# Kernel tuning notes

Measured on AMD Instinct MI355X. Metric: run time of the kernel, lower is better.

## Reference

```python
import jax, jax.numpy as jnp
from jax import lax
import numpy as np

NUM_CLASSES = 7
EDGE_LO, EDGE_HI = 2, 7  # edge_classes = [2,3,4,5,6]
FOCAL_W, DICE_W, BOUND_W, TOPO_W = 0.3, 0.3, 0.2, 0.2
GAMMA = 2.0


def _dwconv(x, k):
    # depthwise 'same' conv with identical spatial kernel per channel
    C = x.shape[1]
    kern = jnp.broadcast_to(k[None, None], (C, 1) + k.shape)
    return lax.conv_general_dilated(
        x, kern, (1, 1), 'SAME',
        dimension_numbers=('NCHW', 'OIHW', 'NCHW'),
        feature_group_count=C)


def setup_inputs() -> dict:
    key = jax.random.key(0)
    k1, k2 = jax.random.split(key)
    logits = jax.random.normal(k1, (8, NUM_CLASSES, 512, 512), dtype=jnp.float32)
    targets = jax.random.randint(k2, (8, 512, 512), 0, NUM_CLASSES, dtype=jnp.int32)
    class_weights = jnp.ones((NUM_CLASSES,), dtype=jnp.float32)
    return {"logits": logits, "targets": targets, "class_weights": class_weights}


def reference(logits, targets, class_weights):
    C = logits.shape[1]
    logp = jax.nn.log_softmax(logits, axis=1)          # [B,C,H,W]
    probs = jnp.exp(logp)
    onehot = (targets[:, None, :, :] == jnp.arange(C)[None, :, None, None]).astype(logits.dtype)

    # ---- Focal loss (weighted CE, pt from the *weighted* CE as in torch code) ----
    nll = -jnp.take_along_axis(logp, targets[:, None].astype(jnp.int32), axis=1)[:, 0]  # [B,H,W]
    ce = class_weights[targets] * nll
    pt = jnp.exp(-ce)
    loss_focal = jnp.mean((1.0 - pt) ** GAMMA * ce)

    # ---- Dice loss (per class, global sums) ----
    inter = jnp.sum(probs * onehot, axis=(0, 2, 3))    # [C]
    union = jnp.sum(probs, axis=(0, 2, 3)) + jnp.sum(onehot, axis=(0, 2, 3))
    loss_dice = jnp.mean(1.0 - (2.0 * inter + 1e-6) / (union + 1e-6))

    # ---- Boundary loss ----
    lap = jnp.array([[0., 1., 0.], [1., -4., 1.], [0., 1., 0.]], dtype=jnp.float32)
    boundary = (jnp.abs(_dwconv(onehot, lap)) > 0).astype(jnp.float32)
    region = _dwconv(boundary, jnp.ones((5, 5), jnp.float32))
    bweight = 1.0 + 4.0 * (region > 0).astype(jnp.float32)
    bce = -onehot * jnp.log(probs + 1e-7) - (1.0 - onehot) * jnp.log(1.0 - probs + 1e-7)
    # sum_c mean_{B,H,W}(bce*w)/C == mean over [B,C,H,W]
    loss_boundary = jnp.mean(bce * bweight)

    # ---- Topology loss (edge classes 2..6) ----
    avg = jnp.ones((3, 3), jnp.float32) / 9.0
    pc = _dwconv(probs[:, EDGE_LO:EDGE_HI], avg)
    tc = _dwconv(onehot[:, EDGE_LO:EDGE_HI], avg)
    diff = jnp.abs(pc - tc)
    mask = onehot[:, EDGE_LO:EDGE_HI]
    msum = jnp.sum(mask, axis=(0, 2, 3))               # [5]
    num = jnp.sum(diff * mask, axis=(0, 2, 3))
    per_cls = jnp.where(msum >= 1.0, num / jnp.maximum(msum, 1.0), 0.0)
    loss_topo = jnp.sum(per_cls) / float(EDGE_HI - EDGE_LO)

    return FOCAL_W * loss_focal + DICE_W * loss_dice + BOUND_W * loss_boundary + TOPO_W * loss_topo
```

## Files before the change

### kernel.cpp

```cpp
#include <hip/hip_runtime.h>

#define BB 8
#define CC 7
#define HH 512
#define WW 512
#define HW (HH*WW)


__global__ __launch_bounds__(256) void main_kernel(const float* __restrict__ logits,
                                                   const int* __restrict__ tgt,
                                                   const float* __restrict__ cw,
                                                   double* __restrict__ acc) {
    __shared__ float sp[1156 * 7];
    __shared__ unsigned char st[38 * 38 + 2];
    __shared__ unsigned char bm[36 * 36 + 4];
    __shared__ unsigned char hm[36 * 32];
    __shared__ float sw[8];
    __shared__ float sred[4 * 28];

    const int tid = threadIdx.x;
    const int b = blockIdx.z;
    const int gx0 = blockIdx.x * 32;
    const int gy0 = blockIdx.y * 32;
    if (tid < 7) sw[tid] = cw[tid];

    const float* lg = logits + (size_t)b * CC * HW;
    const int* tg = tgt + (size_t)b * HW;

    for (int p = tid; p < 1444; p += 256) {
        int iy = p / 38, ix = p - iy * 38;
        int y = gy0 - 3 + iy, x = gx0 - 3 + ix;
        int tv = 255;
        if ((unsigned)y < HH && (unsigned)x < WW) tv = tg[y * WW + x];
        st[p] = (unsigned char)tv;
    }
    __syncthreads();

    for (int p = tid; p < 1296; p += 256) {
        int by = p / 36, bx = p - by * 36;
        int y = gy0 - 2 + by, x = gx0 - 2 + bx;
        unsigned bits = 0;
        if ((unsigned)y < HH && (unsigned)x < WW) {
            int si = (by + 1) * 38 + (bx + 1);
            int t = st[si];
            unsigned orm = 0; int nfirst = -1, same = 1, ninb = 0;
            int n;
            n = st[si - 38]; if (n != 255) { orm |= 1u << n; if (nfirst < 0) nfirst = n; else same &= (n == nfirst); ninb++; }
            n = st[si + 38]; if (n != 255) { orm |= 1u << n; if (nfirst < 0) nfirst = n; else same &= (n == nfirst); ninb++; }
            n = st[si - 1];  if (n != 255) { orm |= 1u << n; if (nfirst < 0) nfirst = n; else same &= (n == nfirst); ninb++; }
            n = st[si + 1];  if (n != 255) { orm |= 1u << n; if (nfirst < 0) nfirst = n; else same &= (n == nfirst); ninb++; }
            unsigned andm = (ninb == 4 && same) ? (1u << nfirst) : 0u;
            unsigned cbit = 1u << t;
            bits = (orm & ~cbit) | (cbit & ~andm);
        }
        bm[p] = (unsigned char)bits;
    }
    __syncthreads();

    for (int p = tid; p < 1152; p += 256) {
        int hy = p >> 5, hx = p & 31;
        const unsigned char* r = &bm[hy * 36 + hx];
        hm[p] = (unsigned char)(r[0] | r[1] | r[2] | r[3] | r[4]);
    }
    __syncthreads();

    for (int p = tid; p < 1156; p += 256) {
        int iy = p / 34, ix = p - iy * 34;
        int y = gy0 - 1 + iy, x = gx0 - 1 + ix;
        float pr[7] = {0,0,0,0,0,0,0};
        if ((unsigned)y < HH && (unsigned)x < WW) {
            const float* lp = lg + y * WW + x;
            float e[7]; float se = 0.f;
#pragma unroll
            for (int c = 0; c < 7; c++) { e[c] = __expf(lp[c * HW]); se += e[c]; }
            float inv = 1.0f / se;
#pragma unroll
            for (int c = 0; c < 7; c++) pr[c] = e[c] * inv;
        }
#pragma unroll
        for (int c = 0; c < 7; c++) sp[p * 7 + c] = pr[c];
    }
    __syncthreads();

    float accF = 0.f, accB = 0.f;
    float sumP[7] = {0,0,0,0,0,0,0};
    float inter[7] = {0,0,0,0,0,0,0};
    float cnt[7] = {0,0,0,0,0,0,0};
    float num[5] = {0,0,0,0,0};

#pragma unroll
    for (int k = 0; k < 4; k++) {
        int p = tid + k * 256;
        int cy = p >> 5, cx = p & 31;
        int hp = (cy + 1) * 34 + (cx + 1);
        int t = st[(cy + 3) * 38 + (cx + 3)];
        float pr[7];
#pragma unroll
        for (int c = 0; c < 7; c++) pr[c] = sp[hp * 7 + c];

        float p_t = sp[hp * 7 + t];
        float ce = sw[t] * (-__logf(p_t));
        float ptv = __expf(-ce);
        float om = 1.0f - ptv;
        accF += om * om * ce;

        const unsigned char* hc = &hm[cy * 32 + cx];
        unsigned rm = (unsigned)(hc[0] | hc[32] | hc[64] | hc[96] | hc[128]);

#pragma unroll
        for (int c = 0; c < 7; c++) {
            float prc = pr[c];
            bool is = (c == t);
            sumP[c] += prc;
            if (is) { inter[c] += prc; cnt[c] += 1.0f; }
            float arg = is ? (prc + 1e-7f) : (1.0f - prc + 1e-7f);
            float bw = 1.0f + 4.0f * (float)((rm >> c) & 1u);
            accB -= bw * __logf(arg);
        }

        if ((unsigned)(t - 2) < 5u) {
            float s = 0.f;
#pragma unroll
            for (int dy = -1; dy <= 1; dy++) {
#pragma unroll
                for (int dx = -1; dx <= 1; dx++) {
                    int np = hp + dy * 34 + dx;
                    float pn = sp[np * 7 + t];
                    int sn = st[(cy + 3 + dy) * 38 + (cx + 3 + dx)];
                    s += pn - ((sn == t) ? 1.0f : 0.0f);
                }
            }
            float val = fabsf(s) * (1.0f / 9.0f);
#pragma unroll
            for (int j = 0; j < 5; j++) num[j] += (t == j + 2) ? val : 0.f;
        }
    }

    float vals[28];
    vals[0] = accF; vals[1] = accB;
#pragma unroll
    for (int c = 0; c < 7; c++) { vals[2+c] = sumP[c]; vals[9+c] = inter[c]; vals[16+c] = cnt[c]; }
#pragma unroll
    for (int j = 0; j < 5; j++) vals[23+j] = num[j];

    int lane = tid & 63, wid = tid >> 6;
#pragma unroll
    for (int i = 0; i < 28; i++) {
        float v = vals[i];
#pragma unroll
        for (int o = 32; o > 0; o >>= 1) v += __shfl_down(v, o, 64);
        if (lane == 0) sred[wid * 28 + i] = v;
    }
    __syncthreads();
    if (tid < 28) {
        float s = sred[tid] + sred[28 + tid] + sred[56 + tid] + sred[84 + tid];
        atomicAdd(&acc[tid], (double)s);
    }
}

__global__ void finalize_kernel(const double* __restrict__ acc, float* __restrict__ out) {
    if (threadIdx.x == 0 && blockIdx.x == 0) {
        double focal = acc[0] / (double)((size_t)BB * HW);
        double bound = acc[1] / (double)((size_t)BB * CC * HW);
        double dice = 0.0;
#pragma unroll
        for (int c = 0; c < 7; c++) {
            double uni = acc[2 + c] + acc[16 + c];
            dice += 1.0 - (2.0 * acc[9 + c] + 1e-6) / (uni + 1e-6);
        }
        dice *= (1.0 / 7.0);
        double topo = 0.0;
#pragma unroll
        for (int j = 0; j < 5; j++) {
            double ms = acc[18 + j];
            double nm = acc[23 + j];
            topo += (ms >= 1.0) ? nm / fmax(ms, 1.0) : 0.0;
        }
        topo *= (1.0 / 5.0);
        out[0] = (float)(0.3 * focal + 0.3 * dice + 0.2 * bound + 0.2 * topo);
    }
}

extern "C" void kernel_launch(void* const* d_in, const int* in_sizes, int n_in,
                              void* d_out, int out_size, void* d_ws, size_t ws_size,
                              hipStream_t stream) {
    const float* logits = (const float*)d_in[0];
    const int* tgt = (const int*)d_in[1];
    const float* cw = (const float*)d_in[2];
    float* out = (float*)d_out;

    double* acc = (double*)d_ws;
    hipMemsetAsync(d_ws, 0, 256, stream);

    dim3 grid(WW / 32, HH / 32, BB);
    main_kernel<<<grid, 256, 0, stream>>>(logits, tgt, cw, acc);
    finalize_kernel<<<1, 64, 0, stream>>>(acc, out);
}
```

Measured before the change: 164.7 us.

## Store probabilities as fp16 in planar LDS layout and alias scratch buffers

Probabilities are stored in shared memory as half precision in a class-planar layout instead of fp32 interleaved. The boundary and dilation scratch buffers are aliased into the same region, and the vertical OR for the boundary mask is precomputed into its own buffer. Together these cut LDS use from roughly 35KB to about 19KB so more blocks can be resident per CU, and the planar layout avoids stride-7 bank access. The cost is fp16 rounding of probabilities, which perturbs the log terms near 0 and 1, plus one extra barrier.

```diff
diff --git a/kernel.cpp b/kernel.cpp
--- a/kernel.cpp
+++ b/kernel.cpp
@@ -1,4 +1,5 @@
 #include <hip/hip_runtime.h>
+#include <hip/hip_fp16.h>
 
 #define BB 8
 #define CC 7
@@ -11,12 +12,14 @@
                                                    const int* __restrict__ tgt,
                                                    const float* __restrict__ cw,
                                                    double* __restrict__ acc) {
-    __shared__ float sp[1156 * 7];
-    __shared__ unsigned char st[38 * 38 + 2];
-    __shared__ unsigned char bm[36 * 36 + 4];
-    __shared__ unsigned char hm[36 * 32];
-    __shared__ float sw[8];
-    __shared__ float sred[4 * 28];
+    __shared__ __align__(16) char smem[19248];
+    unsigned short* sp = (unsigned short*)smem;
+    unsigned char* st = (unsigned char*)(smem + 16296);
+    unsigned char* rm = (unsigned char*)(smem + 17744);
+    float* sw = (float*)(smem + 18768);
+    float* sred = (float*)(smem + 18800);
+    unsigned char* bm = (unsigned char*)smem;
+    unsigned char* hm = (unsigned char*)(smem + 1296);
 
     const int tid = threadIdx.x;
     const int b = blockIdx.z;
@@ -64,6 +67,15 @@
     }
     __syncthreads();
 
+#pragma unroll
+    for (int k = 0; k < 4; k++) {
+        int p = tid + k * 256;
+        int cy = p >> 5, cx = p & 31;
+        const unsigned char* hc = &hm[cy * 32 + cx];
+        rm[p] = (unsigned char)(hc[0] | hc[32] | hc[64] | hc[96] | hc[128]);
+    }
+    __syncthreads();
+
     for (int p = tid; p < 1156; p += 256) {
         int iy = p / 34, ix = p - iy * 34;
         int y = gy0 - 1 + iy, x = gx0 - 1 + ix;
@@ -78,7 +90,8 @@
             for (int c = 0; c < 7; c++) pr[c] = e[c] * inv;
         }
 #pragma unroll
-        for (int c = 0; c < 7; c++) sp[p * 7 + c] = pr[c];
+        for (int c = 0; c < 7; c++)
+            sp[c * 1164 + p] = __half_as_ushort(__float2half_rn(pr[c]));
     }
     __syncthreads();
 
@@ -96,17 +109,18 @@
         int t = st[(cy + 3) * 38 + (cx + 3)];
         float pr[7];
 #pragma unroll
-        for (int c = 0; c < 7; c++) pr[c] = sp[hp * 7 + c];
-
-        float p_t = sp[hp * 7 + t];
+        for (int c = 0; c < 7; c++)
+            pr[c] = __half2float(__ushort_as_half(sp[c * 1164 + hp]));
+
+        float p_t = pr[0];
+#pragma unroll
+        for (int c = 1; c < 7; c++) p_t = (t == c) ? pr[c] : p_t;
         float ce = sw[t] * (-__logf(p_t));
         float ptv = __expf(-ce);
         float om = 1.0f - ptv;
         accF += om * om * ce;
 
-        const unsigned char* hc = &hm[cy * 32 + cx];
-        unsigned rm = (unsigned)(hc[0] | hc[32] | hc[64] | hc[96] | hc[128]);
-
+        unsigned rmv = rm[p];
 #pragma unroll
         for (int c = 0; c < 7; c++) {
             float prc = pr[c];
@@ -114,18 +128,19 @@
             sumP[c] += prc;
             if (is) { inter[c] += prc; cnt[c] += 1.0f; }
             float arg = is ? (prc + 1e-7f) : (1.0f - prc + 1e-7f);
-            float bw = 1.0f + 4.0f * (float)((rm >> c) & 1u);
+            float bw = 1.0f + 4.0f * (float)((rmv >> c) & 1u);
             accB -= bw * __logf(arg);
         }
 
         if ((unsigned)(t - 2) < 5u) {
+            int pl = t * 1164;
             float s = 0.f;
 #pragma unroll
             for (int dy = -1; dy <= 1; dy++) {
 #pragma unroll
                 for (int dx = -1; dx <= 1; dx++) {
                     int np = hp + dy * 34 + dx;
-                    float pn = sp[np * 7 + t];
+                    float pn = __half2float(__ushort_as_half(sp[pl + np]));
                     int sn = st[(cy + 3 + dy) * 38 + (cx + 3 + dx)];
                     s += pn - ((sn == t) ? 1.0f : 0.0f);
                 }
```

After: 166.9 us. No clear change (+1.4%).

## Vectorize logits/target loads, keep interior probs in registers, fp16 edge-class planes

Applied to the files above, without the earlier changes.

Loads logits and targets as float4/int4 per thread, keeping each thread's four interior pixels' softmax results in registers instead of round-tripping all seven channels through shared memory. Only edge classes 2..6 are written to shared memory, as fp16 planes with a padded layout, for the 3x3 topology stencil. The boundary BCE replaces per-class logs with products so only two logs are taken per pixel. Risks are fp16 rounding in the topology term, lost precision from multiplying seven factors before the log, and higher register pressure.

```diff
diff --git a/kernel.cpp b/kernel.cpp
--- a/kernel.cpp
+++ b/kernel.cpp
@@ -1,4 +1,5 @@
 #include <hip/hip_runtime.h>
+#include <hip/hip_fp16.h>
 
 #define BB 8
 #define CC 7
@@ -7,32 +8,159 @@
 #define HW (HH*WW)
 
 
+__device__ __forceinline__ void softmax7x4(float4 a[7]) {
+#pragma unroll
+    for (int c = 0; c < 7; c++) {
+        a[c].x = __expf(a[c].x); a[c].y = __expf(a[c].y);
+        a[c].z = __expf(a[c].z); a[c].w = __expf(a[c].w);
+    }
+    float4 se = a[0];
+#pragma unroll
+    for (int c = 1; c < 7; c++) { se.x += a[c].x; se.y += a[c].y; se.z += a[c].z; se.w += a[c].w; }
+    float ix = 1.f/se.x, iy = 1.f/se.y, iz = 1.f/se.z, iw = 1.f/se.w;
+#pragma unroll
+    for (int c = 0; c < 7; c++) { a[c].x *= ix; a[c].y *= iy; a[c].z *= iz; a[c].w *= iw; }
+}
+
+__device__ __forceinline__ void write_planes(unsigned short* sp, const float4 a[7], int r, int cI) {
+#pragma unroll
+    for (int c = 2; c < 7; c++) {
+        unsigned lo = (unsigned)__half_as_ushort(__float2half_rn(a[c].x))
+                    | ((unsigned)__half_as_ushort(__float2half_rn(a[c].y)) << 16);
+        unsigned hi = (unsigned)__half_as_ushort(__float2half_rn(a[c].z))
+                    | ((unsigned)__half_as_ushort(__float2half_rn(a[c].w)) << 16);
+        uint2 w2 = make_uint2(lo, hi);
+        *(uint2*)&sp[(c - 2) * 1360 + r * 40 + cI * 4] = w2;
+    }
+}
+
+__device__ __forceinline__ void pixel_body(const float pr[7], int t, unsigned rmv,
+                                           const unsigned short* sp, const unsigned char* st,
+                                           const float* sw, int cy, int cx,
+                                           float& accF, float& accB,
+                                           float* sumP, float* inter, float* cnt, float* num) {
+    float p_t = pr[0];
+#pragma unroll
+    for (int c = 1; c < 7; c++) p_t = (t == c) ? pr[c] : p_t;
+    float ce = sw[t] * (-__logf(p_t));
+    float ptv = __expf(-ce);
+    float om = 1.0f - ptv;
+    accF += om * om * ce;
+
+    float prodA = 1.0f, prodB = 1.0f;
+#pragma unroll
+    for (int c = 0; c < 7; c++) {
+        float p = pr[c];
+        bool is = (c == t);
+        sumP[c] += p;
+        if (is) { inter[c] += p; cnt[c] += 1.0f; }
+        float arg = is ? (p + 1e-7f) : (1.0f - p + 1e-7f);
+        prodA *= arg;
+        prodB *= ((rmv >> c) & 1u) ? arg : 1.0f;
+    }
+    accB -= __logf(prodA) + 4.0f * __logf(prodB);
+
+    if ((unsigned)(t - 2) < 5u) {
+        const unsigned short* pl = sp + (t - 2) * 1360;
+        int base = (cy + 1) * 40 + (cx + 4);
+        int sb = (cy + 3) * 40 + (cx + 4);
+        float s = 0.f;
+#pragma unroll
+        for (int dy = -1; dy <= 1; dy++) {
+#pragma unroll
+            for (int dx = -1; dx <= 1; dx++) {
+                float pn = __half2float(__ushort_as_half(pl[base + dy * 40 + dx]));
+                s += pn - ((st[sb + dy * 40 + dx] == t) ? 1.0f : 0.0f);
+            }
+        }
+        float val = fabsf(s) * (1.0f / 9.0f);
+#pragma unroll
+        for (int q = 0; q < 5; q++) num[q] += (t == q + 2) ? val : 0.f;
+    }
+}
+
 __global__ __launch_bounds__(256) void main_kernel(const float* __restrict__ logits,
                                                    const int* __restrict__ tgt,
                                                    const float* __restrict__ cw,
                                                    double* __restrict__ acc) {
-    __shared__ float sp[1156 * 7];
-    __shared__ unsigned char st[38 * 38 + 2];
-    __shared__ unsigned char bm[36 * 36 + 4];
+    __shared__ unsigned short sp[5 * 1360];
+    __shared__ unsigned char st[40 * 38];
+    __shared__ unsigned char bm[36 * 36];
     __shared__ unsigned char hm[36 * 32];
+    __shared__ unsigned char rm[1024];
     __shared__ float sw[8];
-    __shared__ float sred[4 * 28];
+    __shared__ float sred[112];
 
     const int tid = threadIdx.x;
     const int b = blockIdx.z;
-    const int gx0 = blockIdx.x * 32;
-    const int gy0 = blockIdx.y * 32;
+    const int gx0 = blockIdx.x * 32, gy0 = blockIdx.y * 32;
     if (tid < 7) sw[tid] = cw[tid];
 
     const float* lg = logits + (size_t)b * CC * HW;
     const int* tg = tgt + (size_t)b * HW;
 
-    for (int p = tid; p < 1444; p += 256) {
-        int iy = p / 38, ix = p - iy * 38;
-        int y = gy0 - 3 + iy, x = gx0 - 3 + ix;
-        int tv = 255;
-        if ((unsigned)y < HH && (unsigned)x < WW) tv = tg[y * WW + x];
-        st[p] = (unsigned char)tv;
+    int4 tv0, tv1; bool tvld0, tvld1;
+    {
+        int r = tid / 10, cI = tid - r * 10;
+        int y = gy0 - 3 + r, xs = gx0 - 4 + cI * 4;
+        tvld0 = ((unsigned)y < HH) && ((unsigned)xs < WW);
+        size_t off = tvld0 ? ((size_t)y * WW + xs) : 0;
+        tv0 = *(const int4*)(tg + off);
+    }
+    {
+        int g = tid + 256; int gc = (g < 380) ? g : 0;
+        int r = gc / 10, cI = gc - r * 10;
+        int y = gy0 - 3 + r, xs = gx0 - 4 + cI * 4;
+        tvld1 = (g < 380) && ((unsigned)y < HH) && ((unsigned)xs < WW);
+        size_t off = tvld1 ? ((size_t)y * WW + xs) : 0;
+        tv1 = *(const int4*)(tg + off);
+    }
+    const int rI = 1 + (tid >> 3), cII = 1 + (tid & 7);
+    float4 aI[7];
+    {
+        const float* p0 = lg + (size_t)(gy0 - 1 + rI) * WW + (gx0 - 4 + cII * 4);
+#pragma unroll
+        for (int c = 0; c < 7; c++) aI[c] = *(const float4*)(p0 + (size_t)c * HW);
+    }
+    float4 aH[7]; bool hvld = false; int hr = 0, hc = 0;
+    if (tid < 84) {
+        if (tid < 10)      { hr = 0;  hc = tid; }
+        else if (tid < 20) { hr = 33; hc = tid - 10; }
+        else { int e = tid - 20; hr = 1 + (e >> 1); hc = (e & 1) ? 9 : 0; }
+        int y = gy0 - 1 + hr, xs = gx0 - 4 + hc * 4;
+        hvld = ((unsigned)y < HH) && ((unsigned)xs < WW);
+        size_t off = hvld ? ((size_t)y * WW + xs) : 0;
+        const float* p0 = lg + off;
+#pragma unroll
+        for (int c = 0; c < 7; c++) aH[c] = *(const float4*)(p0 + (size_t)c * HW);
+    }
+
+    {
+        int r = tid / 10, cI = tid - r * 10;
+        unsigned w = tvld0 ? ((unsigned)tv0.x | ((unsigned)tv0.y << 8) |
+                              ((unsigned)tv0.z << 16) | ((unsigned)tv0.w << 24))
+                           : 0xFFFFFFFFu;
+        *(unsigned*)&st[r * 40 + cI * 4] = w;
+    }
+    if (tid + 256 < 380) {
+        int g = tid + 256;
+        int r = g / 10, cI = g - r * 10;
+        unsigned w = tvld1 ? ((unsigned)tv1.x | ((unsigned)tv1.y << 8) |
+                              ((unsigned)tv1.z << 16) | ((unsigned)tv1.w << 24))
+                           : 0xFFFFFFFFu;
+        *(unsigned*)&st[r * 40 + cI * 4] = w;
+    }
+
+    softmax7x4(aI);
+    write_planes(sp, aI, rI, cII);
+    if (tid < 84) {
+        if (hvld) {
+            softmax7x4(aH);
+        } else {
+#pragma unroll
+            for (int c = 0; c < 7; c++) aH[c] = make_float4(0.f, 0.f, 0.f, 0.f);
+        }
+        write_planes(sp, aH, hr, hc);
     }
     __syncthreads();
 
@@ -41,12 +169,12 @@
         int y = gy0 - 2 + by, x = gx0 - 2 + bx;
         unsigned bits = 0;
         if ((unsigned)y < HH && (unsigned)x < WW) {
-            int si = (by + 1) * 38 + (bx + 1);
+            int si = (by + 1) * 40 + (bx + 2);
             int t = st[si];
             unsigned orm = 0; int nfirst = -1, same = 1, ninb = 0;
             int n;
-            n = st[si - 38]; if (n != 255) { orm |= 1u << n; if (nfirst < 0) nfirst = n; else same &= (n == nfirst); ninb++; }
-            n = st[si + 38]; if (n != 255) { orm |= 1u << n; if (nfirst < 0) nfirst = n; else same &= (n == nfirst); ninb++; }
+            n = st[si - 40]; if (n != 255) { orm |= 1u << n; if (nfirst < 0) nfirst = n; else same &= (n == nfirst); ninb++; }
+            n = st[si + 40]; if (n != 255) { orm |= 1u << n; if (nfirst < 0) nfirst = n; else same &= (n == nfirst); ninb++; }
             n = st[si - 1];  if (n != 255) { orm |= 1u << n; if (nfirst < 0) nfirst = n; else same &= (n == nfirst); ninb++; }
             n = st[si + 1];  if (n != 255) { orm |= 1u << n; if (nfirst < 0) nfirst = n; else same &= (n == nfirst); ninb++; }
             unsigned andm = (ninb == 4 && same) ? (1u << nfirst) : 0u;
@@ -56,29 +184,17 @@
         bm[p] = (unsigned char)bits;
     }
     __syncthreads();
-
     for (int p = tid; p < 1152; p += 256) {
         int hy = p >> 5, hx = p & 31;
         const unsigned char* r = &bm[hy * 36 + hx];
         hm[p] = (unsigned char)(r[0] | r[1] | r[2] | r[3] | r[4]);
     }
     __syncthreads();
-
-    for (int p = tid; p < 1156; p += 256) {
-        int iy = p / 34, ix = p - iy * 34;
-        int y = gy0 - 1 + iy, x = gx0 - 1 + ix;
-        float pr[7] = {0,0,0,0,0,0,0};
-        if ((unsigned)y < HH && (unsigned)x < WW) {
-            const float* lp = lg + y * WW + x;
-            float e[7]; float se = 0.f;
-#pragma unroll
-            for (int c = 0; c < 7; c++) { e[c] = __expf(lp[c * HW]); se += e[c]; }
-            float inv = 1.0f / se;
-#pragma unroll
-            for (int c = 0; c < 7; c++) pr[c] = e[c] * inv;
-        }
-#pragma unroll
-        for (int c = 0; c < 7; c++) sp[p * 7 + c] = pr[c];
+#pragma unroll
+    for (int k = 0; k < 4; k++) {
+        int p = tid + k * 256;
+        const unsigned char* hc2 = &hm[(p >> 5) * 32 + (p & 31)];
+        rm[p] = (unsigned char)(hc2[0] | hc2[32] | hc2[64] | hc2[96] | hc2[128]);
     }
     __syncthreads();
 
@@ -87,53 +203,28 @@
     float inter[7] = {0,0,0,0,0,0,0};
     float cnt[7] = {0,0,0,0,0,0,0};
     float num[5] = {0,0,0,0,0};
-
-#pragma unroll
-    for (int k = 0; k < 4; k++) {
-        int p = tid + k * 256;
-        int cy = p >> 5, cx = p & 31;
-        int hp = (cy + 1) * 34 + (cx + 1);
-        int t = st[(cy + 3) * 38 + (cx + 3)];
-        float pr[7];
-#pragma unroll
-        for (int c = 0; c < 7; c++) pr[c] = sp[hp * 7 + c];
-
-        float p_t = sp[hp * 7 + t];
-        float ce = sw[t] * (-__logf(p_t));
-        float ptv = __expf(-ce);
-        float om = 1.0f - ptv;
-        accF += om * om * ce;
-
-        const unsigned char* hc = &hm[cy * 32 + cx];
-        unsigned rm = (unsigned)(hc[0] | hc[32] | hc[64] | hc[96] | hc[128]);
-
-#pragma unroll
-        for (int c = 0; c < 7; c++) {
-            float prc = pr[c];
-            bool is = (c == t);
-            sumP[c] += prc;
-            if (is) { inter[c] += prc; cnt[c] += 1.0f; }
-            float arg = is ? (prc + 1e-7f) : (1.0f - prc + 1e-7f);
-            float bw = 1.0f + 4.0f * (float)((rm >> c) & 1u);
-            accB -= bw * __logf(arg);
-        }
-
-        if ((unsigned)(t - 2) < 5u) {
-            float s = 0.f;
-#pragma unroll
-            for (int dy = -1; dy <= 1; dy++) {
-#pragma unroll
-                for (int dx = -1; dx <= 1; dx++) {
-                    int np = hp + dy * 34 + dx;
-                    float pn = sp[np * 7 + t];
-                    int sn = st[(cy + 3 + dy) * 38 + (cx + 3 + dx)];
-                    s += pn - ((sn == t) ? 1.0f : 0.0f);
-                }
-            }
-            float val = fabsf(s) * (1.0f / 9.0f);
-#pragma unroll
-            for (int j = 0; j < 5; j++) num[j] += (t == j + 2) ? val : 0.f;
-        }
+    const int cy = tid >> 3, cxb = (tid & 7) * 4;
+    unsigned rmv4 = *(unsigned*)&rm[cy * 32 + cxb];
+    unsigned t4 = *(unsigned*)&st[(cy + 3) * 40 + cxb + 4];
+    {
+        float pr[7] = {aI[0].x, aI[1].x, aI[2].x, aI[3].x, aI[4].x, aI[5].x, aI[6].x};
+        pixel_body(pr, (int)(t4 & 255u), rmv4 & 255u, sp, st, sw, cy, cxb + 0,
+                   accF, accB, sumP, inter, cnt, num);
+    }
+    {
+        float pr[7] = {aI[0].y, aI[1].y, aI[2].y, aI[3].y, aI[4].y, aI[5].y, aI[6].y};
+        pixel_body(pr, (int)((t4 >> 8) & 255u), (rmv4 >> 8) & 255u, sp, st, sw, cy, cxb + 1,
+                   accF, accB, sumP, inter, cnt, num);
+    }
+    {
+        float pr[7] = {aI[0].z, aI[1].z, aI[2].z, aI[3].z, aI[4].z, aI[5].z, aI[6].z};
+        pixel_body(pr, (int)((t4 >> 16) & 255u), (rmv4 >> 16) & 255u, sp, st, sw, cy, cxb + 2,
+                   accF, accB, sumP, inter, cnt, num);
+    }
+    {
+        float pr[7] = {aI[0].w, aI[1].w, aI[2].w, aI[3].w, aI[4].w, aI[5].w, aI[6].w};
+        pixel_body(pr, (int)((t4 >> 24) & 255u), (rmv4 >> 24) & 255u, sp, st, sw, cy, cxb + 3,
+                   accF, accB, sumP, inter, cnt, num);
     }
 
     float vals[28];
```

Result: no change. 164.2 us (-0.3%).
